# Kernel tuning notes

Hardware: AMD Instinct MI355X
Metric: run time of the kernel (lower is better)

Reference implementation:

```python
import jax, jax.numpy as jnp
import numpy as np

B, H, W, D, C = 8, 128, 128, 64, 16

def setup_inputs() -> dict:
    key = jax.random.key(0)
    k1, k2 = jax.random.split(key)
    inputs = jax.random.uniform(k1, (B, H, W, D), dtype=jnp.float32)
    beta = jax.random.normal(k2, (D, C), dtype=jnp.float32) * 0.05  # 'random_normal' init
    return {"inputs": inputs, "beta": beta}

def reference(inputs, beta):
    # u[i, c] = beta[i,c]^2 / sum_c beta[i,c]^2   (row-normalized squared weights)
    b2 = jnp.square(beta)                               # [D, C]
    u = b2 / jnp.sum(b2, axis=1, keepdims=True)         # [D, C]
    # mass_prototype[b,h,w,i,c] = u[i,c] * inputs[b,h,w,i]
    # Single fused broadcast multiply replacing the original nested concat loops.
    return inputs[..., None] * u                        # [B, H, W, D, C]
```

## Files before the change

kernel.cpp:

```cpp
#include <hip/hip_runtime.h>


#define Dd 64
#define Cc 16

__global__ __launch_bounds__(256) void DS2_62466004353281_kernel(
    const float* __restrict__ inputs,
    const float* __restrict__ beta,
    float* __restrict__ out,
    int n_quads)
{
    __shared__ float u[Dd * Cc];
    const int t = threadIdx.x;

    if (t < Dd) {
        float b2[Cc];
        float s = 0.f;
#pragma unroll
        for (int c = 0; c < Cc; ++c) {
            float b = beta[t * Cc + c];
            b2[c] = b * b;
            s += b2[c];
        }
        float inv = 1.0f / s;
#pragma unroll
        for (int c = 0; c < Cc; ++c) u[t * Cc + c] = b2[c] * inv;
    }
    __syncthreads();

    const float4* __restrict__ u4 = (const float4*)u;
    float4* __restrict__ out4 = (float4*)out;

    const int stride = gridDim.x * blockDim.x;
    for (int idx = blockIdx.x * blockDim.x + t; idx < n_quads; idx += stride) {
        const int elem = idx >> 2;
        const int q    = idx & 3;
        const int i    = elem & (Dd - 1);
        const float x  = inputs[elem];
        const float4 uu = u4[i * 4 + q];
        float4 o;
        o.x = x * uu.x;
        o.y = x * uu.y;
        o.z = x * uu.z;
        o.w = x * uu.w;
        out4[idx] = o;
    }
}

extern "C" void kernel_launch(void* const* d_in, const int* in_sizes, int n_in,
                              void* d_out, int out_size, void* d_ws, size_t ws_size,
                              hipStream_t stream) {
    const float* inputs = (const float*)d_in[0];
    const float* beta   = (const float*)d_in[1];
    float* out          = (float*)d_out;

    const int n_quads = out_size / 4;
    dim3 grid(8192), block(256);
    DS2_62466004353281_kernel<<<grid, block, 0, stream>>>(inputs, beta, out, n_quads);
}
```

Baseline: 556.6 us.

## Hoist invariant u load and software-pipeline input loads across unrolled batches

The u value each thread needs is now loaded once, relying on the grid stride being a multiple of 256 so the channel index stays fixed per thread. The grid shrinks to 2048 blocks, and each thread prefetches input values two unrolled batches ahead in registers before issuing its float4 stores. The goal is to take the shared-memory lookup and load latency off the store path of this write-bound kernel, at the cost of more registers and a fallback path for sizes that do not divide evenly.

```diff
diff --git a/kernel.cpp b/kernel.cpp
--- a/kernel.cpp
+++ b/kernel.cpp
@@ -3,6 +3,7 @@
 
 #define Dd 64
 #define Cc 16
+#define UNR 8
 
 __global__ __launch_bounds__(256) void DS2_62466004353281_kernel(
     const float* __restrict__ inputs,
@@ -31,19 +32,68 @@
     const float4* __restrict__ u4 = (const float4*)u;
     float4* __restrict__ out4 = (float4*)out;
 
-    const int stride = gridDim.x * blockDim.x;
-    for (int idx = blockIdx.x * blockDim.x + t; idx < n_quads; idx += stride) {
-        const int elem = idx >> 2;
-        const int q    = idx & 3;
-        const int i    = elem & (Dd - 1);
-        const float x  = inputs[elem];
-        const float4 uu = u4[i * 4 + q];
-        float4 o;
-        o.x = x * uu.x;
-        o.y = x * uu.y;
-        o.z = x * uu.z;
-        o.w = x * uu.w;
-        out4[idx] = o;
+    const int stride  = gridDim.x * blockDim.x;
+    const int estride = stride >> 2;
+    const int base    = blockIdx.x * blockDim.x + t;
+
+    const float4 uu = u4[(((base >> 2) & (Dd - 1)) << 2) | (base & 3)];
+
+    if ((n_quads % stride) == 0 && ((n_quads / stride) % UNR) == 0 &&
+        (n_quads / stride) >= 2 * UNR) {
+        const int nb = (n_quads / stride) / UNR;
+
+        float x0[UNR], x1[UNR];
+        int le   = base >> 2;
+        int sidx = base;
+
+#pragma unroll
+        for (int k = 0; k < UNR; ++k) x0[k] = inputs[le + k * estride];
+        le += UNR * estride;
+#pragma unroll
+        for (int k = 0; k < UNR; ++k) x1[k] = inputs[le + k * estride];
+        le += UNR * estride;
+
+        for (int b = 0; b < nb - 2; ++b) {
+            float xn[UNR];
+#pragma unroll
+            for (int k = 0; k < UNR; ++k) xn[k] = inputs[le + k * estride];
+            le += UNR * estride;
+
+#pragma unroll
+            for (int k = 0; k < UNR; ++k) {
+                const float x = x0[k];
+                float4 o;
+                o.x = x * uu.x; o.y = x * uu.y; o.z = x * uu.z; o.w = x * uu.w;
+                out4[sidx + k * stride] = o;
+            }
+            sidx += UNR * stride;
+
+#pragma unroll
+            for (int k = 0; k < UNR; ++k) { x0[k] = x1[k]; x1[k] = xn[k]; }
+        }
+
+#pragma unroll
+        for (int k = 0; k < UNR; ++k) {
+            const float x = x0[k];
+            float4 o;
+            o.x = x * uu.x; o.y = x * uu.y; o.z = x * uu.z; o.w = x * uu.w;
+            out4[sidx + k * stride] = o;
+        }
+        sidx += UNR * stride;
+#pragma unroll
+        for (int k = 0; k < UNR; ++k) {
+            const float x = x1[k];
+            float4 o;
+            o.x = x * uu.x; o.y = x * uu.y; o.z = x * uu.z; o.w = x * uu.w;
+            out4[sidx + k * stride] = o;
+        }
+    } else {
+        for (int idx = base; idx < n_quads; idx += stride) {
+            const float x = inputs[idx >> 2];
+            float4 o;
+            o.x = x * uu.x; o.y = x * uu.y; o.z = x * uu.z; o.w = x * uu.w;
+            out4[idx] = o;
+        }
     }
 }
 
@@ -55,6 +105,6 @@
     float* out          = (float*)d_out;
 
     const int n_quads = out_size / 4;
-    dim3 grid(8192), block(256);
+    dim3 grid(2048), block(256);
     DS2_62466004353281_kernel<<<grid, block, 0, stream>>>(inputs, beta, out, n_quads);
 }
```

After: 563.4 us. Within noise of the previous version (+1.2%).
